# Performance work log

Hardware: AMD Instinct MI355X
Metric: run time of the kernel (lower is better)

Reference implementation:

```python
import jax, jax.numpy as jnp
import numpy as np
from jax import lax

K = 7  # kernel_size
PAD = K // 2


def _feature_difference(t):
    # t: [B, C, H, W] -> normalized census-style local differences [B, K*K, H, W]
    intensity = t.mean(axis=1, keepdims=True)  # [B,1,H,W]
    # Equivalent to conv2d with the identity (eye) kernel in the torch module:
    # channel k gathers the neighbor at offset (k//K, k%K) with zero padding.
    patches = lax.conv_general_dilated_patches(
        intensity, filter_shape=(K, K), window_strides=(1, 1),
        padding=[(PAD, PAD), (PAD, PAD)])  # [B, K*K, H, W]
    local_diff = patches - intensity
    return local_diff / jnp.sqrt(0.81 + local_diff * local_diff)


def setup_inputs() -> dict:
    key = jax.random.key(0)
    kx, ky = jax.random.split(key)
    B, C, H, W = 8, 3, 320, 1024
    x = jax.random.uniform(kx, (B, C, H, W), dtype=jnp.float32)
    y = jax.random.uniform(ky, (B, C, H, W), dtype=jnp.float32)
    return {"x": x, "y": y}


def reference(x, y):
    diff_x = _feature_difference(x)
    diff_y = _feature_difference(y)
    diff_total = diff_x - lax.stop_gradient(diff_y)  # .detach() on y branch
    d2 = diff_total * diff_total
    dist = (d2 / (0.1 + d2)).mean(axis=1, keepdims=True)  # [B,1,H,W]
    b, c, h, w = x.shape
    # valid-region mask: ones in the interior, zeros in the PAD-wide border
    mask = jnp.zeros((b, 1, h, w), dtype=x.dtype)
    mask = mask.at[:, :, PAD:h - PAD, PAD:w - PAD].set(1.0)
    return (dist * mask).mean()
```

## Files before the change

kernel.cpp:

```cpp
#include <hip/hip_runtime.h>

#define KSZ 7
#define PAD 3
#define HH 320
#define WW 1024
#define BB 8
#define TH 32
#define TW 64
#define HALO_H (TH + 2*PAD)
#define HALO_W (TW + 2*PAD)
#define LDS_W  72

#define OUT_SCALE (1.0f / (49.0f * (float)(BB) * (float)(HH) * (float)(WW)))

__global__ __launch_bounds__(256) void ternary_loss_kernel(
    const float* __restrict__ x, const float* __restrict__ y,
    float* __restrict__ out)
{
    __shared__ float sIx[HALO_H][LDS_W];
    __shared__ float sIy[HALO_H][LDS_W];
    __shared__ float wave_sums[4];

    const int tile_j = blockIdx.x * TW;
    const int tile_i = blockIdx.y * TH;
    const int b      = blockIdx.z;
    const int tx  = threadIdx.x;
    const int ty  = threadIdx.y;
    const int tid = ty * 64 + tx;

    const float* xb = x + (size_t)b * 3 * HH * WW;
    const float* yb = y + (size_t)b * 3 * HH * WW;

    for (int idx = tid; idx < HALO_H * HALO_W; idx += 256) {
        int r = idx / HALO_W;
        int c = idx - r * HALO_W;
        int gi = tile_i - PAD + r;
        int gj = tile_j - PAD + c;
        float vx = 0.0f, vy = 0.0f;
        if (gi >= 0 && gi < HH && gj >= 0 && gj < WW) {
            size_t o = (size_t)gi * WW + gj;
            vx = (xb[o] + xb[(size_t)HH * WW + o] + xb[2 * (size_t)HH * WW + o]) * (1.0f / 3.0f);
            vy = (yb[o] + yb[(size_t)HH * WW + o] + yb[2 * (size_t)HH * WW + o]) * (1.0f / 3.0f);
        }
        sIx[r][c] = vx;
        sIy[r][c] = vy;
    }
    __syncthreads();

    const int gj = tile_j + tx;
    float colOK[7];
    #pragma unroll
    for (int d = 0; d < 7; ++d) {
        int nj = gj + d - 3;
        colOK[d] = (nj >= PAD && nj < WW - PAD) ? 1.0f : 0.0f;
    }

    float acc = 0.0f;

    #pragma unroll 1
    for (int k = 0; k < TH / 4; ++k) {
        const int li = ty + 4 * k;
        const int gi = tile_i + li;

        const float cx = sIx[li + PAD][tx + PAD];
        const float cy = sIy[li + PAD][tx + PAD];

        const float mc = (gi >= PAD && gi < HH - PAD && colOK[3] > 0.5f) ? 1.0f : 0.0f;

        float rowOK[4];
        #pragma unroll
        for (int di = 0; di < 4; ++di) {
            int ni = gi + di;
            rowOK[di] = (ni >= PAD && ni < HH - PAD) ? 1.0f : 0.0f;
        }

        #pragma unroll
        for (int di = 0; di <= 3; ++di) {
            #pragma unroll
            for (int dj = -3; dj <= 3; ++dj) {
                if (di == 0 && dj <= 0) continue;
                float nx = sIx[li + PAD + di][tx + PAD + dj];
                float ny = sIy[li + PAD + di][tx + PAD + dj];
                float dx = nx - cx;
                float gx = dx * __builtin_amdgcn_rsqf(fmaf(dx, dx, 0.81f));
                float dy = ny - cy;
                float gy = dy * __builtin_amdgcn_rsqf(fmaf(dy, dy, 0.81f));
                float t  = gx - gy;
                float t2 = t * t;
                float v  = t2 * __builtin_amdgcn_rcpf(t2 + 0.1f);
                float w  = mc + rowOK[di] * colOK[dj + 3];
                acc = fmaf(v, w, acc);
            }
        }
    }

    #pragma unroll
    for (int off = 32; off > 0; off >>= 1)
        acc += __shfl_down(acc, off, 64);
    if (tx == 0) wave_sums[ty] = acc;
    __syncthreads();
    if (tid == 0) {
        float total = wave_sums[0] + wave_sums[1] + wave_sums[2] + wave_sums[3];
        atomicAdd(out, total * OUT_SCALE);
    }
}

extern "C" void kernel_launch(void* const* d_in, const int* in_sizes, int n_in,
                              void* d_out, int out_size, void* d_ws, size_t ws_size,
                              hipStream_t stream) {
    const float* x = (const float*)d_in[0];
    const float* y = (const float*)d_in[1];
    float* out = (float*)d_out;

    hipMemsetAsync(out, 0, sizeof(float), stream);

    dim3 grid(WW / TW, HH / TH, BB);
    dim3 block(64, 4, 1);
    ternary_loss_kernel<<<grid, block, 0, stream>>>(x, y, out);
}
```

Baseline: 130.7 us.

## Use a register sliding window and fold the loss term into a constant

Each wave now owns a contiguous band of 8 rows and keeps a rotating 4-row by 7-column window of x and y intensities in registers. Each new row is loaded from LDS once instead of re-reading every neighbor from LDS. The loss term t²/(t²+0.1) is rewritten as 1 − 0.1/(t²+0.1); the constant part is added once as a precomputed total from one block, which removes a multiply per pair. The trade-offs are higher register pressure and a risk of float cancellation in the final sum.

```diff
diff --git a/kernel.cpp b/kernel.cpp
--- a/kernel.cpp
+++ b/kernel.cpp
@@ -1,6 +1,5 @@
 #include <hip/hip_runtime.h>
 
-#define KSZ 7
 #define PAD 3
 #define HH 320
 #define WW 1024
@@ -10,8 +9,12 @@
 #define HALO_H (TH + 2*PAD)
 #define HALO_W (TW + 2*PAD)
 #define LDS_W  72
+#define RPW 8
 
-#define OUT_SCALE (1.0f / (49.0f * (float)(BB) * (float)(HH) * (float)(WW)))
+#define NIN ((HH - 2*PAD) * (WW - 2*PAD))
+#define OUT_SCALE (1.0 / (49.0 * (double)BB * (double)HH * (double)WW))
+#define C0 ((float)(48.0 * (double)BB * (double)NIN * OUT_SCALE))
+#define NEG_SCALE ((float)(-0.1 * OUT_SCALE))
 
 __global__ __launch_bounds__(256) void ternary_loss_kernel(
     const float* __restrict__ x, const float* __restrict__ y,
@@ -25,8 +28,8 @@
     const int tile_i = blockIdx.y * TH;
     const int b      = blockIdx.z;
     const int tx  = threadIdx.x;
-    const int ty  = threadIdx.y;
-    const int tid = ty * 64 + tx;
+    const int wv  = threadIdx.y;
+    const int tid = wv * 64 + tx;
 
     const float* xb = x + (size_t)b * 3 * HH * WW;
     const float* yb = y + (size_t)b * 3 * HH * WW;
@@ -55,41 +58,62 @@
         colOK[d] = (nj >= PAD && nj < WW - PAD) ? 1.0f : 0.0f;
     }
 
+    const int li0 = wv * RPW;
+
+    float wx[4][7], wy[4][7];
+    #pragma unroll
+    for (int r = 0; r < 3; ++r) {
+        #pragma unroll
+        for (int d = 0; d < 7; ++d) {
+            wx[r][d] = sIx[li0 + 3 + r][tx + d];
+            wy[r][d] = sIy[li0 + 3 + r][tx + d];
+        }
+    }
+
     float acc = 0.0f;
 
     #pragma unroll 1
-    for (int k = 0; k < TH / 4; ++k) {
-        const int li = ty + 4 * k;
-        const int gi = tile_i + li;
+    for (int io = 0; io < RPW / 4; ++io) {
+        #pragma unroll
+        for (int iu = 0; iu < 4; ++iu) {
+            const int li = li0 + io * 4 + iu;
+            const int gi = tile_i + li;
+            const int snew = (iu + 3) & 3;
+            #pragma unroll
+            for (int d = 0; d < 7; ++d) {
+                wx[snew][d] = sIx[li + 6][tx + d];
+                wy[snew][d] = sIy[li + 6][tx + d];
+            }
 
-        const float cx = sIx[li + PAD][tx + PAD];
-        const float cy = sIy[li + PAD][tx + PAD];
+            float rin[4];
+            #pragma unroll
+            for (int di = 0; di < 4; ++di) {
+                int ni = gi + di;
+                rin[di] = (ni >= PAD && ni < HH - PAD) ? 1.0f : 0.0f;
+            }
+            const float mc = rin[0] * colOK[3];
 
-        const float mc = (gi >= PAD && gi < HH - PAD && colOK[3] > 0.5f) ? 1.0f : 0.0f;
+            const float cx = wx[iu & 3][3];
+            const float cy = wy[iu & 3][3];
 
-        float rowOK[4];
-        #pragma unroll
-        for (int di = 0; di < 4; ++di) {
-            int ni = gi + di;
-            rowOK[di] = (ni >= PAD && ni < HH - PAD) ? 1.0f : 0.0f;
-        }
-
-        #pragma unroll
-        for (int di = 0; di <= 3; ++di) {
             #pragma unroll
-            for (int dj = -3; dj <= 3; ++dj) {
-                if (di == 0 && dj <= 0) continue;
-                float nx = sIx[li + PAD + di][tx + PAD + dj];
-                float ny = sIy[li + PAD + di][tx + PAD + dj];
-                float dx = nx - cx;
-                float gx = dx * __builtin_amdgcn_rsqf(fmaf(dx, dx, 0.81f));
-                float dy = ny - cy;
-                float gy = dy * __builtin_amdgcn_rsqf(fmaf(dy, dy, 0.81f));
-                float t  = gx - gy;
-                float t2 = t * t;
-                float v  = t2 * __builtin_amdgcn_rcpf(t2 + 0.1f);
-                float w  = mc + rowOK[di] * colOK[dj + 3];
-                acc = fmaf(v, w, acc);
+            for (int di = 0; di <= 3; ++di) {
+                const int s = (iu + di) & 3;
+                #pragma unroll
+                for (int dj = -3; dj <= 3; ++dj) {
+                    if (di == 0 && dj <= 0) continue;
+                    float nx = wx[s][dj + 3];
+                    float ny = wy[s][dj + 3];
+                    float dx = nx - cx;
+                    float gx = dx * __builtin_amdgcn_rsqf(fmaf(dx, dx, 0.81f));
+                    float dy = ny - cy;
+                    float gy = dy * __builtin_amdgcn_rsqf(fmaf(dy, dy, 0.81f));
+                    float t  = gx - gy;
+                    float denom = fmaf(t, t, 0.1f);
+                    float r = __builtin_amdgcn_rcpf(denom);
+                    float w = fmaf(rin[di], colOK[dj + 3], mc);
+                    acc = fmaf(w, r, acc);
+                }
             }
         }
     }
@@ -97,11 +121,13 @@
     #pragma unroll
     for (int off = 32; off > 0; off >>= 1)
         acc += __shfl_down(acc, off, 64);
-    if (tx == 0) wave_sums[ty] = acc;
+    if (tx == 0) wave_sums[wv] = acc;
     __syncthreads();
     if (tid == 0) {
-        float total = wave_sums[0] + wave_sums[1] + wave_sums[2] + wave_sums[3];
-        atomicAdd(out, total * OUT_SCALE);
+        float total = (wave_sums[0] + wave_sums[1] + wave_sums[2] + wave_sums[3]) * NEG_SCALE;
+        if (blockIdx.x == 0 && blockIdx.y == 0 && blockIdx.z == 0)
+            total += C0;
+        atomicAdd(out, total);
     }
 }
 
```

Result: faster. 125.9 us (-3.7%).
